# Kernel optimization log

Measured on AMD Instinct MI355X. Metric: run time of the kernel, lower is better.

Reference implementation:

```python
import jax, jax.numpy as jnp
import numpy as np

BIG = 1e8  # replaces inf entries in the cost matrix, as in the torch module


def _hungarian(cost):
    """Min-cost bipartite assignment for an (n, m) cost matrix with n <= m.
    Returns, for each row i, the assigned column (same optimum as
    scipy.optimize.linear_sum_assignment; rows come back in sorted order).
    Classic O(n*m^2) shortest-augmenting-path algorithm with potentials."""
    n, m = cost.shape
    INF = np.inf
    u = np.zeros(n + 1)
    v = np.zeros(m + 1)
    p = np.zeros(m + 1, dtype=np.int64)   # p[j]: row matched to col j (1-based; 0 = free)
    way = np.zeros(m + 1, dtype=np.int64)
    for i in range(1, n + 1):
        p[0] = i
        j0 = 0
        minv = np.full(m + 1, INF)
        used = np.zeros(m + 1, dtype=bool)
        while True:
            used[j0] = True
            i0 = p[j0]
            cur = cost[i0 - 1, :] - u[i0] - v[1:]
            free = ~used[1:]
            better = free & (cur < minv[1:])
            minv[1:] = np.where(better, cur, minv[1:])
            way[1:] = np.where(better, j0, way[1:])
            cand = np.where(free, minv[1:], INF)
            j1 = int(np.argmin(cand)) + 1
            delta = cand[j1 - 1]
            u[p[used]] += delta
            v[used] -= delta
            minv[~used] -= delta
            j0 = j1
            if p[j0] == 0:
                break
        while j0 != 0:
            j1 = int(way[j0])
            p[j0] = p[j1]
            j0 = j1
    ans = np.zeros(n, dtype=np.int64)
    for j in range(1, m + 1):
        if p[j] != 0:
            ans[p[j] - 1] = j - 1
    return ans


def _matched_labels(outputs, gold, weight):
    """Per-sample Hungarian matching on the restricted-softmax NLL cost,
    exactly as the torch module: cost[b] = -log_softmax(outputs[b][:, gold[b]], 1) * w[gold[b]].
    Matching is detached (host-side), mirroring scipy linear_sum_assignment."""
    B, S, C = outputs.shape
    idx = jnp.broadcast_to(gold[:, None, :], (B, S, S))
    sub = jnp.take_along_axis(outputs, idx, axis=2)                  # [B,S,S] logits at gold cols
    cost = -jax.nn.log_softmax(sub, axis=2) * weight[gold][:, None, :]
    cost = jnp.where(jnp.isinf(cost), BIG, cost)
    cost_np = np.asarray(cost, dtype=np.float64)
    gold_np = np.asarray(gold)
    match = np.empty_like(gold_np)
    for b in range(B):
        col = _hungarian(cost_np[b])                                 # row i -> gold column
        match[b] = gold_np[b][col]
    return jnp.asarray(match)


def setup_inputs() -> dict:
    key = jax.random.key(0)
    k1, k2 = jax.random.split(key)
    B, S, C = 128, 20, 32000
    outputs = jax.random.normal(k1, (B, S, C), dtype=jnp.float32)
    gold_label_ids = jax.random.randint(k2, (B, S), 0, C)
    mask = jnp.ones((B, S), dtype=bool)
    weight = jnp.ones((C,), dtype=jnp.float32)
    return {"outputs": outputs, "gold_label_ids": gold_label_ids, "mask": mask, "weight": weight}


def reference(outputs, gold_label_ids, mask, weight):
    eps = 1e-8
    match = _matched_labels(outputs, gold_label_ids, weight)         # [B,S] matched class ids
    logp = jax.nn.log_softmax(outputs, axis=-1)                      # [B,S,C]
    nll = -jnp.take_along_axis(logp, match[..., None], axis=2)[..., 0] * weight[match]
    m = mask.reshape(-1).astype(outputs.dtype)
    loss = nll.reshape(-1) * m
    return jnp.sum(loss) / (jnp.sum(m) + eps)
```

## Files before the change

kernel.cpp:

```cpp
#include <hip/hip_runtime.h>
#include <hip/hip_bf16.h>
#include <math.h>

#define NB 128
#define NS 20
#define NC 32000
#define RPB 2
#define NLSE (NB * NS / RPB)
#define NBLOCKS (NB + NLSE)

static __device__ __forceinline__ float fmin_x1(float x) {
    int t = __builtin_amdgcn_update_dpp(0, __float_as_int(x), 0xB1, 0xf, 0xf, true);
    return fminf(x, __int_as_float(t));
}
static __device__ __forceinline__ float fmin_x2(float x) {
    int t = __builtin_amdgcn_update_dpp(0, __float_as_int(x), 0x4E, 0xf, 0xf, true);
    return fminf(x, __int_as_float(t));
}
static __device__ __forceinline__ float fmin_x4(float x) {
    int t = __builtin_amdgcn_ds_swizzle(__float_as_int(x), 0x101F);
    return fminf(x, __int_as_float(t));
}
static __device__ __forceinline__ float fmin_x8(float x) {
    int t = __builtin_amdgcn_ds_swizzle(__float_as_int(x), 0x201F);
    return fminf(x, __int_as_float(t));
}
static __device__ __forceinline__ float fmin_x16(float x) {
    int t = __builtin_amdgcn_ds_swizzle(__float_as_int(x), 0x401F);
    return fminf(x, __int_as_float(t));
}
static __device__ __forceinline__ float readlane_f(float x, int lane) {
    return __int_as_float(__builtin_amdgcn_readlane(__float_as_int(x), lane));
}

__global__ __launch_bounds__(256) void mega_kernel(
        const float* __restrict__ outputs,
        const int* __restrict__ gold,
        const float* __restrict__ weight,
        int* __restrict__ match_col,
        float* __restrict__ sub_ws,
        float* __restrict__ logZ) {

    if (blockIdx.x < NB) {
        const int b = blockIdx.x;
        const int* g = gold + b * NS;
        __shared__ float cst[NS * NS];
        __shared__ float lzs[NS];

        for (int e = threadIdx.x; e < NS * NS; e += 256) {
            int i = e / NS, j = e - i * NS;
            float x = outputs[(size_t)(b * NS + i) * NC + g[j]];
            cst[e] = x;
            sub_ws[(size_t)(b * NS + i) * NS + j] = x;
        }
        __syncthreads();
        if (threadIdx.x < NS) {
            int i = threadIdx.x;
            float mx = cst[i * NS];
#pragma unroll
            for (int j = 1; j < NS; ++j) mx = fmaxf(mx, cst[i * NS + j]);
            float s = 0.f;
#pragma unroll
            for (int j = 0; j < NS; ++j) s += __expf(cst[i * NS + j] - mx);
            lzs[i] = mx + __logf(s);
        }
        __syncthreads();
        for (int e = threadIdx.x; e < NS * NS; e += 256) {
            int i = e / NS, j = e - i * NS;
            float c = -(cst[e] - lzs[i]) * weight[g[j]];
            if (isinf(c)) c = 1e8f;
            cst[e] = c;
        }
        __syncthreads();
        if (threadIdx.x >= 64) return;

        const int lane = threadIdx.x;
        const float FINF = INFINITY;
        float up_j = 0.f;
        float v_j = 0.f;
        int p_j = 0;
        int way_j = 0;
        const bool is_col = (lane >= 1 && lane <= NS);

        for (int i = 1; i <= NS; ++i) {
            if (lane == 0) { p_j = i; up_j = 0.f; }
            int j0 = 0;
            float minv_j = FINF;
            bool used_j = false;
            while (true) {
                int pp = __builtin_amdgcn_readlane(p_j, j0);
                if (pp == 0) break;
                if (lane == j0) used_j = true;
                float upp = readlane_f(up_j, j0);
                float cv = cst[is_col ? (pp - 1) * NS + (lane - 1) : 0];
                if (is_col && !used_j) {
                    float cur = cv - upp - v_j;
                    if (cur < minv_j) { minv_j = cur; way_j = j0; }
                }
                float cand = (is_col && !used_j) ? minv_j : FINF;
                float mval = fmin_x16(fmin_x8(fmin_x4(fmin_x2(fmin_x1(cand)))));
                unsigned long long bal = __ballot(cand == mval) & 0xFFFFFFFFull;
                int j1 = __ffsll(bal) - 1;
                float delta = mval;
                if (used_j) { up_j += delta; v_j -= delta; }
                else if (is_col) minv_j -= delta;
                j0 = j1;
            }
            while (j0 != 0) {
                int   j1   = __builtin_amdgcn_readlane(way_j, j0);
                int   pj1  = __builtin_amdgcn_readlane(p_j, j1);
                float upj1 = readlane_f(up_j, j1);
                if (lane == j0) { p_j = pj1; up_j = upj1; }
                j0 = j1;
            }
        }
        if (is_col && p_j != 0) {
            match_col[b * NS + (p_j - 1)] = lane - 1;
        }
    } else {
        __shared__ float smx[4], ssm[4];
        const int rbase = (blockIdx.x - NB) * RPB;
        for (int rr = 0; rr < RPB; ++rr) {
            const int row = rbase + rr;
            const float4* rp = (const float4*)(outputs + (size_t)row * NC);
            const int n4 = NC / 4;

            float m = -INFINITY;
            float s = 0.f;
            for (int idx = threadIdx.x; idx < n4; idx += blockDim.x) {
                float4 x = rp[idx];
                float m4 = fmaxf(fmaxf(x.x, x.y), fmaxf(x.z, x.w));
                float nm = fmaxf(m, m4);
                s = s * __expf(m - nm)
                  + __expf(x.x - nm) + __expf(x.y - nm)
                  + __expf(x.z - nm) + __expf(x.w - nm);
                m = nm;
            }
            for (int off = 1; off < 64; off <<= 1) {
                float om = __shfl_xor(m, off);
                float os = __shfl_xor(s, off);
                float nm = fmaxf(m, om);
                s = s * __expf(m - nm) + os * __expf(om - nm);
                m = nm;
            }
            __syncthreads();
            int wid = threadIdx.x >> 6;
            if ((threadIdx.x & 63) == 0) { smx[wid] = m; ssm[wid] = s; }
            __syncthreads();
            if (threadIdx.x == 0) {
                float M = smx[0], S = ssm[0];
                for (int w = 1; w < 4; ++w) {
                    float om = smx[w], os = ssm[w];
                    float nm = fmaxf(M, om);
                    S = S * __expf(M - nm) + os * __expf(om - nm);
                    M = nm;
                }
                logZ[row] = M + __logf(S);
            }
        }
    }
}

__global__ __launch_bounds__(256) void final_kernel(
        const int* __restrict__ match_col,
        const float* __restrict__ sub_ws,
        const float* __restrict__ logZ,
        const float* __restrict__ weight,
        const int* __restrict__ gold,
        const unsigned char* __restrict__ mask,
        float* __restrict__ out) {
    double nsum = 0.0, msum = 0.0;
    for (int r = threadIdx.x; r < NB * NS; r += 256) {
        int b = r / NS;
        int col = match_col[r];
        float x = sub_ws[(size_t)r * NS + col];
        float w = weight[gold[b * NS + col]];
        float nll = -(x - logZ[r]) * w;
        float mk = mask[r] ? 1.f : 0.f;
        nsum += (double)(nll * mk);
        msum += (double)mk;
    }
    for (int off = 1; off < 64; off <<= 1) {
        nsum += __shfl_xor(nsum, off);
        msum += __shfl_xor(msum, off);
    }
    __shared__ double sn[4], sm[4];
    int wid = threadIdx.x >> 6;
    if ((threadIdx.x & 63) == 0) { sn[wid] = nsum; sm[wid] = msum; }
    __syncthreads();
    if (threadIdx.x == 0) {
        double N = 0.0, M = 0.0;
        for (int w = 0; w < 4; ++w) { N += sn[w]; M += sm[w]; }
        out[0] = (float)(N / (M + 1e-8));
    }
}

extern "C" void kernel_launch(void* const* d_in, const int* in_sizes, int n_in,
                              void* d_out, int out_size, void* d_ws, size_t ws_size,
                              hipStream_t stream) {
    const float* outputs        = (const float*)d_in[0];
    const int*   gold           = (const int*)d_in[1];
    const unsigned char* mask   = (const unsigned char*)d_in[2];
    const float* weight         = (const float*)d_in[3];
    float* out = (float*)d_out;

    char* ws = (char*)d_ws;
    int*   match_col = (int*)ws;
    float* logZ      = (float*)(ws + (size_t)NB * NS * 4);
    float* sub_ws    = (float*)(ws + (size_t)NB * NS * 8);

    mega_kernel<<<NBLOCKS, 256, 0, stream>>>(outputs, gold, weight,
                                             match_col, sub_ws, logZ);
    final_kernel<<<1, 256, 0, stream>>>(match_col, sub_ws, logZ, weight, gold,
                                        mask, out);
}
```

Measured before the change: 73.34 us.

## Use atomic work-stealing over quarter-row LSE chunks shared with Hungarian blocks

Replaces the fixed two-rows-per-block logsumexp blocks with a persistent grid of 2048 blocks. Each block pulls quarter-row chunks from a global atomic counter, and the Hungarian blocks join the pool once their matching is done. Partial max/sum pairs are written per chunk and merged in the final kernel. The aim is better load balance and more memory-level parallelism, with four float4 loads issued up front per thread. The cost is an extra memset, one atomic per chunk, and more partial-result traffic.

```diff
diff --git a/kernel.cpp b/kernel.cpp
--- a/kernel.cpp
+++ b/kernel.cpp
@@ -5,9 +5,11 @@
 #define NB 128
 #define NS 20
 #define NC 32000
-#define RPB 2
-#define NLSE (NB * NS / RPB)
-#define NBLOCKS (NB + NLSE)
+#define NROWS (NB * NS)
+#define CPR 4
+#define NCHUNK (NROWS * CPR)
+#define CHUNK_F4 2000
+#define NBLOCKS 2048
 
 static __device__ __forceinline__ float fmin_x1(float x) {
     int t = __builtin_amdgcn_update_dpp(0, __float_as_int(x), 0xB1, 0xf, 0xf, true);
@@ -37,9 +39,14 @@
         const float* __restrict__ outputs,
         const int* __restrict__ gold,
         const float* __restrict__ weight,
+        unsigned* __restrict__ ctr,
         int* __restrict__ match_col,
         float* __restrict__ sub_ws,
-        float* __restrict__ logZ) {
+        float* __restrict__ pm,
+        float* __restrict__ ps) {
+
+    __shared__ float smx[4], ssm[4];
+    __shared__ unsigned cur;
 
     if (blockIdx.x < NB) {
         const int b = blockIdx.x;
@@ -72,91 +79,113 @@
             cst[e] = c;
         }
         __syncthreads();
-        if (threadIdx.x >= 64) return;
-
-        const int lane = threadIdx.x;
-        const float FINF = INFINITY;
-        float up_j = 0.f;
-        float v_j = 0.f;
-        int p_j = 0;
-        int way_j = 0;
-        const bool is_col = (lane >= 1 && lane <= NS);
-
-        for (int i = 1; i <= NS; ++i) {
-            if (lane == 0) { p_j = i; up_j = 0.f; }
-            int j0 = 0;
-            float minv_j = FINF;
-            bool used_j = false;
-            while (true) {
-                int pp = __builtin_amdgcn_readlane(p_j, j0);
-                if (pp == 0) break;
-                if (lane == j0) used_j = true;
-                float upp = readlane_f(up_j, j0);
-                float cv = cst[is_col ? (pp - 1) * NS + (lane - 1) : 0];
-                if (is_col && !used_j) {
-                    float cur = cv - upp - v_j;
-                    if (cur < minv_j) { minv_j = cur; way_j = j0; }
+
+        if (threadIdx.x < 64) {
+            const int lane = threadIdx.x;
+            const float FINF = INFINITY;
+            float up_j = 0.f, v_j = 0.f;
+            int p_j = 0, way_j = 0;
+            const bool is_col = (lane >= 1 && lane <= NS);
+
+            for (int i = 1; i <= NS; ++i) {
+                if (lane == 0) { p_j = i; up_j = 0.f; }
+                int j0 = 0;
+                float minv_j = FINF;
+                bool used_j = false;
+                while (true) {
+                    int pp = __builtin_amdgcn_readlane(p_j, j0);
+                    if (pp == 0) break;
+                    if (lane == j0) used_j = true;
+                    float upp = readlane_f(up_j, j0);
+                    float cv = cst[is_col ? (pp - 1) * NS + (lane - 1) : 0];
+                    if (is_col && !used_j) {
+                        float curv = cv - upp - v_j;
+                        if (curv < minv_j) { minv_j = curv; way_j = j0; }
+                    }
+                    float cand = (is_col && !used_j) ? minv_j : FINF;
+                    float mval = fmin_x16(fmin_x8(fmin_x4(fmin_x2(fmin_x1(cand)))));
+                    unsigned long long bal = __ballot(cand == mval) & 0xFFFFFFFFull;
+                    int j1 = __ffsll(bal) - 1;
+                    float delta = mval;
+                    if (used_j) { up_j += delta; v_j -= delta; }
+                    else if (is_col) minv_j -= delta;
+                    j0 = j1;
                 }
-                float cand = (is_col && !used_j) ? minv_j : FINF;
-                float mval = fmin_x16(fmin_x8(fmin_x4(fmin_x2(fmin_x1(cand)))));
-                unsigned long long bal = __ballot(cand == mval) & 0xFFFFFFFFull;
-                int j1 = __ffsll(bal) - 1;
-                float delta = mval;
-                if (used_j) { up_j += delta; v_j -= delta; }
-                else if (is_col) minv_j -= delta;
-                j0 = j1;
+                while (j0 != 0) {
+                    int   j1   = __builtin_amdgcn_readlane(way_j, j0);
+                    int   pj1  = __builtin_amdgcn_readlane(p_j, j1);
+                    float upj1 = readlane_f(up_j, j1);
+                    if (lane == j0) { p_j = pj1; up_j = upj1; }
+                    j0 = j1;
+                }
             }
-            while (j0 != 0) {
-                int   j1   = __builtin_amdgcn_readlane(way_j, j0);
-                int   pj1  = __builtin_amdgcn_readlane(p_j, j1);
-                float upj1 = readlane_f(up_j, j1);
-                if (lane == j0) { p_j = pj1; up_j = upj1; }
-                j0 = j1;
+            if (is_col && p_j != 0) {
+                match_col[b * NS + (p_j - 1)] = lane - 1;
             }
         }
-        if (is_col && p_j != 0) {
-            match_col[b * NS + (p_j - 1)] = lane - 1;
-        }
-    } else {
-        __shared__ float smx[4], ssm[4];
-        const int rbase = (blockIdx.x - NB) * RPB;
-        for (int rr = 0; rr < RPB; ++rr) {
-            const int row = rbase + rr;
-            const float4* rp = (const float4*)(outputs + (size_t)row * NC);
-            const int n4 = NC / 4;
-
-            float m = -INFINITY;
-            float s = 0.f;
-            for (int idx = threadIdx.x; idx < n4; idx += blockDim.x) {
-                float4 x = rp[idx];
-                float m4 = fmaxf(fmaxf(x.x, x.y), fmaxf(x.z, x.w));
-                float nm = fmaxf(m, m4);
-                s = s * __expf(m - nm)
-                  + __expf(x.x - nm) + __expf(x.y - nm)
-                  + __expf(x.z - nm) + __expf(x.w - nm);
-                m = nm;
+        __syncthreads();
+    }
+
+    for (;;) {
+        __syncthreads();
+        if (threadIdx.x == 0) {
+            cur = __hip_atomic_fetch_add(ctr, 1u, __ATOMIC_RELAXED,
+                                         __HIP_MEMORY_SCOPE_AGENT);
+        }
+        __syncthreads();
+        unsigned c = cur;
+        if (c >= (unsigned)NCHUNK) break;
+        const int row = c >> 2, q = c & 3;
+        const float4* rp = (const float4*)outputs
+                         + (size_t)row * (NC / 4) + q * CHUNK_F4;
+
+        float m = -INFINITY;
+        float s = 0.f;
+        {
+            int i0 = threadIdx.x;
+            float4 a = rp[i0];
+            float4 bq = rp[i0 + 256];
+            float4 cq = rp[i0 + 512];
+            float4 d = rp[i0 + 768];
+            float m4 = fmaxf(fmaxf(fmaxf(a.x, a.y), fmaxf(a.z, a.w)),
+                             fmaxf(fmaxf(bq.x, bq.y), fmaxf(bq.z, bq.w)));
+            m4 = fmaxf(m4, fmaxf(fmaxf(fmaxf(cq.x, cq.y), fmaxf(cq.z, cq.w)),
+                                 fmaxf(fmaxf(d.x, d.y), fmaxf(d.z, d.w))));
+            m = m4;
+            s = __expf(a.x - m) + __expf(a.y - m) + __expf(a.z - m) + __expf(a.w - m)
+              + __expf(bq.x - m) + __expf(bq.y - m) + __expf(bq.z - m) + __expf(bq.w - m)
+              + __expf(cq.x - m) + __expf(cq.y - m) + __expf(cq.z - m) + __expf(cq.w - m)
+              + __expf(d.x - m) + __expf(d.y - m) + __expf(d.z - m) + __expf(d.w - m);
+        }
+        for (int idx = 1024 + threadIdx.x; idx < CHUNK_F4; idx += 256) {
+            float4 x = rp[idx];
+            float m4 = fmaxf(fmaxf(x.x, x.y), fmaxf(x.z, x.w));
+            float nm = fmaxf(m, m4);
+            s = s * __expf(m - nm)
+              + __expf(x.x - nm) + __expf(x.y - nm)
+              + __expf(x.z - nm) + __expf(x.w - nm);
+            m = nm;
+        }
+        for (int off = 1; off < 64; off <<= 1) {
+            float om = __shfl_xor(m, off);
+            float os = __shfl_xor(s, off);
+            float nm = fmaxf(m, om);
+            s = s * __expf(m - nm) + os * __expf(om - nm);
+            m = nm;
+        }
+        int wid = threadIdx.x >> 6;
+        if ((threadIdx.x & 63) == 0) { smx[wid] = m; ssm[wid] = s; }
+        __syncthreads();
+        if (threadIdx.x == 0) {
+            float M = smx[0], S = ssm[0];
+            for (int w = 1; w < 4; ++w) {
+                float om = smx[w], os = ssm[w];
+                float nm = fmaxf(M, om);
+                S = S * __expf(M - nm) + os * __expf(om - nm);
+                M = nm;
             }
-            for (int off = 1; off < 64; off <<= 1) {
-                float om = __shfl_xor(m, off);
-                float os = __shfl_xor(s, off);
-                float nm = fmaxf(m, om);
-                s = s * __expf(m - nm) + os * __expf(om - nm);
-                m = nm;
-            }
-            __syncthreads();
-            int wid = threadIdx.x >> 6;
-            if ((threadIdx.x & 63) == 0) { smx[wid] = m; ssm[wid] = s; }
-            __syncthreads();
-            if (threadIdx.x == 0) {
-                float M = smx[0], S = ssm[0];
-                for (int w = 1; w < 4; ++w) {
-                    float om = smx[w], os = ssm[w];
-                    float nm = fmaxf(M, om);
-                    S = S * __expf(M - nm) + os * __expf(om - nm);
-                    M = nm;
-                }
-                logZ[row] = M + __logf(S);
-            }
+            pm[c] = M;
+            ps[c] = S;
         }
     }
 }
@@ -164,18 +193,28 @@
 __global__ __launch_bounds__(256) void final_kernel(
         const int* __restrict__ match_col,
         const float* __restrict__ sub_ws,
-        const float* __restrict__ logZ,
+        const float* __restrict__ pm,
+        const float* __restrict__ ps,
         const float* __restrict__ weight,
         const int* __restrict__ gold,
         const unsigned char* __restrict__ mask,
         float* __restrict__ out) {
     double nsum = 0.0, msum = 0.0;
-    for (int r = threadIdx.x; r < NB * NS; r += 256) {
+    for (int r = threadIdx.x; r < NROWS; r += 256) {
+        float M = pm[r * CPR], S = ps[r * CPR];
+#pragma unroll
+        for (int q = 1; q < CPR; ++q) {
+            float om = pm[r * CPR + q], os = ps[r * CPR + q];
+            float nm = fmaxf(M, om);
+            S = S * __expf(M - nm) + os * __expf(om - nm);
+            M = nm;
+        }
+        float lz = M + __logf(S);
         int b = r / NS;
         int col = match_col[r];
         float x = sub_ws[(size_t)r * NS + col];
         float w = weight[gold[b * NS + col]];
-        float nll = -(x - logZ[r]) * w;
+        float nll = -(x - lz) * w;
         float mk = mask[r] ? 1.f : 0.f;
         nsum += (double)(nll * mk);
         msum += (double)mk;
@@ -205,12 +244,16 @@
     float* out = (float*)d_out;
 
     char* ws = (char*)d_ws;
-    int*   match_col = (int*)ws;
-    float* logZ      = (float*)(ws + (size_t)NB * NS * 4);
-    float* sub_ws    = (float*)(ws + (size_t)NB * NS * 8);
-
-    mega_kernel<<<NBLOCKS, 256, 0, stream>>>(outputs, gold, weight,
-                                             match_col, sub_ws, logZ);
-    final_kernel<<<1, 256, 0, stream>>>(match_col, sub_ws, logZ, weight, gold,
-                                        mask, out);
-}
+    unsigned* ctr     = (unsigned*)ws;
+    int*   match_col  = (int*)(ws + 16);
+    float* sub_ws     = (float*)(ws + 16 + (size_t)NROWS * 4);
+    float* pm         = (float*)(ws + 16 + (size_t)NROWS * 4
+                                 + (size_t)NROWS * NS * 4);
+    float* ps         = pm + NCHUNK;
+
+    hipMemsetAsync(ctr, 0, sizeof(unsigned), stream);
+    mega_kernel<<<NBLOCKS, 256, 0, stream>>>(outputs, gold, weight, ctr,
+                                             match_col, sub_ws, pm, ps);
+    final_kernel<<<1, 256, 0, stream>>>(match_col, sub_ws, pm, ps, weight,
+                                        gold, mask, out);
+}
```

Measured after the change: 173.3 us. 2.36x slower.

## Split LSE rows into per-wave chunks with unrolled loads and merge partials in final kernel

Applied to the files above, without the earlier changes.

The row log-sum-exp work is now split so that each wave processes a quarter of a row. Loads are unrolled four-wide per iteration to keep more memory requests in flight, and the block-level shared-memory reductions and barriers are gone. Partial max and sum values are written to the workspace and merged in the final kernel, which now runs 1024 threads. This costs extra partial-result traffic and a little more work in the single-block final kernel.

```diff
diff --git a/kernel.cpp b/kernel.cpp
--- a/kernel.cpp
+++ b/kernel.cpp
@@ -5,9 +5,12 @@
 #define NB 128
 #define NS 20
 #define NC 32000
-#define RPB 2
-#define NLSE (NB * NS / RPB)
-#define NBLOCKS (NB + NLSE)
+#define NROWS (NB * NS)
+#define CPR 4
+#define NCHUNK (NROWS * CPR)
+#define CHUNK_F4 2000
+#define NQB (NCHUNK / 4)
+#define NBLOCKS (NB + NQB)
 
 static __device__ __forceinline__ float fmin_x1(float x) {
     int t = __builtin_amdgcn_update_dpp(0, __float_as_int(x), 0xB1, 0xf, 0xf, true);
@@ -31,6 +34,9 @@
 }
 static __device__ __forceinline__ float readlane_f(float x, int lane) {
     return __int_as_float(__builtin_amdgcn_readlane(__float_as_int(x), lane));
+}
+static __device__ __forceinline__ float max4(float4 a) {
+    return fmaxf(fmaxf(a.x, a.y), fmaxf(a.z, a.w));
 }
 
 __global__ __launch_bounds__(256) void mega_kernel(
@@ -39,10 +45,13 @@
         const float* __restrict__ weight,
         int* __restrict__ match_col,
         float* __restrict__ sub_ws,
-        float* __restrict__ logZ) {
-
-    if (blockIdx.x < NB) {
-        const int b = blockIdx.x;
+        float* __restrict__ pm,
+        float* __restrict__ ps) {
+
+    const int bid = blockIdx.x;
+
+    if (bid < NB) {
+        const int b = bid;
         const int* g = gold + b * NS;
         __shared__ float cst[NS * NS];
         __shared__ float lzs[NS];
@@ -76,10 +85,8 @@
 
         const int lane = threadIdx.x;
         const float FINF = INFINITY;
-        float up_j = 0.f;
-        float v_j = 0.f;
-        int p_j = 0;
-        int way_j = 0;
+        float up_j = 0.f, v_j = 0.f;
+        int p_j = 0, way_j = 0;
         const bool is_col = (lane >= 1 && lane <= NS);
 
         for (int i = 1; i <= NS; ++i) {
@@ -94,8 +101,8 @@
                 float upp = readlane_f(up_j, j0);
                 float cv = cst[is_col ? (pp - 1) * NS + (lane - 1) : 0];
                 if (is_col && !used_j) {
-                    float cur = cv - upp - v_j;
-                    if (cur < minv_j) { minv_j = cur; way_j = j0; }
+                    float curv = cv - upp - v_j;
+                    if (curv < minv_j) { minv_j = curv; way_j = j0; }
                 }
                 float cand = (is_col && !used_j) ? minv_j : FINF;
                 float mval = fmin_x16(fmin_x8(fmin_x4(fmin_x2(fmin_x1(cand)))));
@@ -118,64 +125,79 @@
             match_col[b * NS + (p_j - 1)] = lane - 1;
         }
     } else {
-        __shared__ float smx[4], ssm[4];
-        const int rbase = (blockIdx.x - NB) * RPB;
-        for (int rr = 0; rr < RPB; ++rr) {
-            const int row = rbase + rr;
-            const float4* rp = (const float4*)(outputs + (size_t)row * NC);
-            const int n4 = NC / 4;
-
-            float m = -INFINITY;
-            float s = 0.f;
-            for (int idx = threadIdx.x; idx < n4; idx += blockDim.x) {
-                float4 x = rp[idx];
-                float m4 = fmaxf(fmaxf(x.x, x.y), fmaxf(x.z, x.w));
-                float nm = fmaxf(m, m4);
-                s = s * __expf(m - nm)
-                  + __expf(x.x - nm) + __expf(x.y - nm)
-                  + __expf(x.z - nm) + __expf(x.w - nm);
-                m = nm;
-            }
-            for (int off = 1; off < 64; off <<= 1) {
-                float om = __shfl_xor(m, off);
-                float os = __shfl_xor(s, off);
-                float nm = fmaxf(m, om);
-                s = s * __expf(m - nm) + os * __expf(om - nm);
-                m = nm;
-            }
-            __syncthreads();
-            int wid = threadIdx.x >> 6;
-            if ((threadIdx.x & 63) == 0) { smx[wid] = m; ssm[wid] = s; }
-            __syncthreads();
-            if (threadIdx.x == 0) {
-                float M = smx[0], S = ssm[0];
-                for (int w = 1; w < 4; ++w) {
-                    float om = smx[w], os = ssm[w];
-                    float nm = fmaxf(M, om);
-                    S = S * __expf(M - nm) + os * __expf(om - nm);
-                    M = nm;
-                }
-                logZ[row] = M + __logf(S);
-            }
-        }
-    }
-}
-
-__global__ __launch_bounds__(256) void final_kernel(
+        const int lane = threadIdx.x & 63;
+        const int wid  = threadIdx.x >> 6;
+        const int chunk = (bid - NB) * 4 + wid;
+        const int row = chunk >> 2, q = chunk & 3;
+        const float4* rp = (const float4*)outputs
+                         + (size_t)row * (NC / 4) + q * CHUNK_F4;
+
+        float m = -INFINITY;
+        float s = 0.f;
+        for (int it = 0; it < 7; ++it) {
+            int i0 = it * 256 + lane;
+            float4 a  = rp[i0];
+            float4 b4 = rp[i0 + 64];
+            float4 c  = rp[i0 + 128];
+            float4 d  = rp[i0 + 192];
+            float m4 = fmaxf(fmaxf(max4(a), max4(b4)), fmaxf(max4(c), max4(d)));
+            float nm = fmaxf(m, m4);
+            float sl = __expf(a.x - nm) + __expf(a.y - nm)
+                     + __expf(a.z - nm) + __expf(a.w - nm)
+                     + __expf(b4.x - nm) + __expf(b4.y - nm)
+                     + __expf(b4.z - nm) + __expf(b4.w - nm)
+                     + __expf(c.x - nm) + __expf(c.y - nm)
+                     + __expf(c.z - nm) + __expf(c.w - nm)
+                     + __expf(d.x - nm) + __expf(d.y - nm)
+                     + __expf(d.z - nm) + __expf(d.w - nm);
+            s = s * __expf(m - nm) + sl;
+            m = nm;
+        }
+        for (int idx = 1792 + lane; idx < CHUNK_F4; idx += 64) {
+            float4 x = rp[idx];
+            float m4 = max4(x);
+            float nm = fmaxf(m, m4);
+            s = s * __expf(m - nm)
+              + __expf(x.x - nm) + __expf(x.y - nm)
+              + __expf(x.z - nm) + __expf(x.w - nm);
+            m = nm;
+        }
+        for (int off = 1; off < 64; off <<= 1) {
+            float om = __shfl_xor(m, off);
+            float os = __shfl_xor(s, off);
+            float nm = fmaxf(m, om);
+            s = s * __expf(m - nm) + os * __expf(om - nm);
+            m = nm;
+        }
+        if (lane == 0) { pm[chunk] = m; ps[chunk] = s; }
+    }
+}
+
+__global__ __launch_bounds__(1024) void final_kernel(
         const int* __restrict__ match_col,
         const float* __restrict__ sub_ws,
-        const float* __restrict__ logZ,
+        const float* __restrict__ pm,
+        const float* __restrict__ ps,
         const float* __restrict__ weight,
         const int* __restrict__ gold,
         const unsigned char* __restrict__ mask,
         float* __restrict__ out) {
     double nsum = 0.0, msum = 0.0;
-    for (int r = threadIdx.x; r < NB * NS; r += 256) {
+    for (int r = threadIdx.x; r < NROWS; r += 1024) {
+        float M = pm[r * CPR], S = ps[r * CPR];
+#pragma unroll
+        for (int q = 1; q < CPR; ++q) {
+            float om = pm[r * CPR + q], os = ps[r * CPR + q];
+            float nm = fmaxf(M, om);
+            S = S * __expf(M - nm) + os * __expf(om - nm);
+            M = nm;
+        }
+        float lz = M + __logf(S);
         int b = r / NS;
         int col = match_col[r];
         float x = sub_ws[(size_t)r * NS + col];
         float w = weight[gold[b * NS + col]];
-        float nll = -(x - logZ[r]) * w;
+        float nll = -(x - lz) * w;
         float mk = mask[r] ? 1.f : 0.f;
         nsum += (double)(nll * mk);
         msum += (double)mk;
@@ -184,13 +206,13 @@
         nsum += __shfl_xor(nsum, off);
         msum += __shfl_xor(msum, off);
     }
-    __shared__ double sn[4], sm[4];
+    __shared__ double sn[16], sm[16];
     int wid = threadIdx.x >> 6;
     if ((threadIdx.x & 63) == 0) { sn[wid] = nsum; sm[wid] = msum; }
     __syncthreads();
     if (threadIdx.x == 0) {
         double N = 0.0, M = 0.0;
-        for (int w = 0; w < 4; ++w) { N += sn[w]; M += sm[w]; }
+        for (int w = 0; w < 16; ++w) { N += sn[w]; M += sm[w]; }
         out[0] = (float)(N / (M + 1e-8));
     }
 }
@@ -206,11 +228,13 @@
 
     char* ws = (char*)d_ws;
     int*   match_col = (int*)ws;
-    float* logZ      = (float*)(ws + (size_t)NB * NS * 4);
-    float* sub_ws    = (float*)(ws + (size_t)NB * NS * 8);
+    float* sub_ws    = (float*)(ws + (size_t)NROWS * 4);
+    float* pm        = (float*)(ws + (size_t)NROWS * 4
+                                + (size_t)NROWS * NS * 4);
+    float* ps        = pm + NCHUNK;
 
     mega_kernel<<<NBLOCKS, 256, 0, stream>>>(outputs, gold, weight,
-                                             match_col, sub_ws, logZ);
-    final_kernel<<<1, 256, 0, stream>>>(match_col, sub_ws, logZ, weight, gold,
-                                        mask, out);
-}
+                                             match_col, sub_ws, pm, ps);
+    final_kernel<<<1, 1024, 0, stream>>>(match_col, sub_ws, pm, ps, weight,
+                                         gold, mask, out);
+}
```

After: 70.04 us. -4.5%, faster.
